# Performance work log

Measured on AMD Instinct MI355X. Metric: run time of the kernel, lower is better.

## Reference

```python
import jax, jax.numpy as jnp
import numpy as np
from math import factorial

LMAX = 8
BATCH = 65536


def _cg(j1, m1, j2, m2, j3, m3):
    """Clebsch-Gordan coefficient <j1 m1 j2 m2 | j3 m3> (Racah formula)."""
    if m1 + m2 != m3:
        return 0.0
    if j3 < abs(j1 - j2) or j3 > j1 + j2:
        return 0.0
    f = factorial
    pre = ((2 * j3 + 1) * f(j1 + j2 - j3) * f(j1 - j2 + j3) * f(-j1 + j2 + j3)
           / f(j1 + j2 + j3 + 1)) ** 0.5
    pre *= (f(j1 + m1) * f(j1 - m1) * f(j2 + m2) * f(j2 - m2)
            * f(j3 + m3) * f(j3 - m3)) ** 0.5
    kmin = max(0, j2 - j3 - m1, j1 - j3 + m2)
    kmax = min(j1 + j2 - j3, j1 - m1, j2 + m2)
    s = 0.0
    for k in range(kmin, kmax + 1):
        s += (-1) ** k / (f(k) * f(j1 + j2 - j3 - k) * f(j1 - m1 - k)
                          * f(j2 + m2 - k) * f(j3 - j2 + m1 + k) * f(j3 - j1 - m2 + k))
    return pre * s


def _cg_tensor(l1, l2, lo):
    C = np.zeros((2 * l1 + 1, 2 * l2 + 1, 2 * lo + 1), dtype=np.float32)
    for i, m1 in enumerate(range(-l1, l1 + 1)):
        for j, m2 in enumerate(range(-l2, l2 + 1)):
            M = m1 + m2
            if abs(M) <= lo:
                C[i, j, M + lo] = _cg(l1, m1, l2, m2, lo, M)
    return jnp.asarray(C)


def _build_full_index_map(lmax):
    im = []
    for l1 in range(lmax + 1):
        for l2 in range(l1, lmax + 1):
            for lv in range(abs(l1 - l2), min(l1 + l2, lmax) + 1):
                im.append((l1, l2, lv))
    return im


def _build_cg_power_index_map(lmax):
    if lmax < 2:
        return []
    entries = []
    for l2 in range(2, lmax + 1):
        lo_min = l2 - 1
        lo_max = min(l2 + 1, lmax)
        entries.append((1, l2, lo_min))
        if l2 >= 4 and lo_min + 1 <= lo_max:
            entries.append((1, l2, lo_min + 1))
    for l2 in range(3, lmax + 1):
        lo_min = l2 - 2
        lo_max = min(l2 + 2, lmax)
        entries.append((2, l2, lo_min))
        if lo_min + 1 <= lo_max:
            entries.append((2, l2, lo_min + 1))
    if lmax >= 3:
        entries.append((3, 3, 2))
    for l2 in range(4, lmax + 1):
        lo_min = l2 - 3
        lo_max = min(l2 + 3, lmax)
        entries.append((3, l2, lo_min))
        if l2 % 2 == 1 and l2 >= 5:
            if lo_min + 1 <= lo_max:
                entries.append((3, l2, lo_min + 1))
            if lo_min + 2 <= lo_max:
                entries.append((3, l2, lo_min + 2))
    return entries


FULL_MAP = _build_full_index_map(LMAX)
POWER_MAP = _build_cg_power_index_map(LMAX)
_CG = {t: _cg_tensor(*t) for t in sorted(set(FULL_MAP) | set(POWER_MAP))}
N_OUT = len(FULL_MAP) + len(POWER_MAP)


def setup_inputs() -> dict:
    k1, k2 = jax.random.split(jax.random.key(0))
    shape = (BATCH, LMAX + 1, LMAX + 1)
    return {
        "coeffs_real": jax.random.normal(k1, shape, dtype=jnp.float32),
        "coeffs_imag": jax.random.normal(k2, shape, dtype=jnp.float32),
    }


def _full_coeffs(c):
    """Extend m>=0 coefficients to full m range: F_l^{-m} = (-1)^m conj(F_l^m)."""
    F = {}
    for l in range(LMAX + 1):
        pos = c[:, l, :l + 1]  # (B, l+1), m = 0..l
        if l == 0:
            F[l] = pos
        else:
            signs = jnp.asarray((-1.0) ** np.arange(1, l + 1), dtype=jnp.float32)
            neg = (signs * jnp.conj(pos[:, 1:]))[:, ::-1]  # m = -l..-1
            F[l] = jnp.concatenate([neg, pos], axis=1)  # (B, 2l+1)
    return F


def reference(coeffs_real, coeffs_imag):
    c = (coeffs_real + 1j * coeffs_imag).astype(jnp.complex64)
    F = _full_coeffs(c)
    outs = []
    # scalar bispectrum entries: beta = sum_{m1,m2} C F1 F2 conj(F_lo^{m1+m2})
    for (l1, l2, lo) in FULL_MAP:
        C = _CG[(l1, l2, lo)]
        G = jnp.einsum('bi,bj,ijk->bk', F[l1], F[l2], C)  # coupled component, (B, 2lo+1)
        beta = jnp.sum(G * jnp.conj(F[lo]), axis=1)
        outs.append(beta.real)
    for (l1, l2, lo) in POWER_MAP:
        C = _CG[(l1, l2, lo)]
        G = jnp.einsum('bi,bj,ijk->bk', F[l1], F[l2], C)
        outs.append(jnp.sum(G.real ** 2 + G.imag ** 2, axis=1))
    return jnp.stack(outs, axis=1)  # (B, N_OUT) float32
```

## Files before the change

### kernel.cpp

```cpp
#include <hip/hip_runtime.h>
#include <utility>

#define LMAX 8
#define NENT 249
#define NPAIR 45
#define EPB 128
#define TPB 512
#define ESTR 130
#define NCO 45
#define PLANE (NCO*ESTR)
#define P1END 30
#define FSPLIT 100
#define PSLOT 115
#define NSLOT 149

typedef __attribute__((ext_vector_type(2))) float f32x2;

struct P2 { int l1, l2; };

__host__ __device__ constexpr int tri_(int l){ return l*(l+1)/2; }
__host__ __device__ constexpr int sr_(int m){ return m>=0 ? 1 : (((-m)&1)? -1 : 1); }
__host__ __device__ constexpr int sq_(int m){ return m>=0 ? 1 : (((-m)&1)? 1 : -1); }

__host__ __device__ constexpr P2 pair_of(int w){
  int n=0;
  for(int a=0;a<=LMAX;a++) for(int b=a;b<=LMAX;b++){ if(n==w) return P2{a,b}; n++; }
  return P2{0,0};
}

__host__ __device__ constexpr int full_rank(int l1,int l2,int lo){
  int r=0;
  for(int a=0;a<=LMAX;a++) for(int b=a;b<=LMAX;b++){
    int hi=a+b>LMAX?LMAX:a+b;
    for(int c=b-a;c<=hi;c++){ if(a==l1&&b==l2&&c==lo) return r; r++; }
  }
  return -1;
}

__host__ __device__ constexpr int power_idx(int l1,int l2,int lo){
  int n=0;
  for(int b=2;b<=LMAX;b++){
    if(l1==1&&l2==b&&lo==b-1) return n; n++;
    if(b>=4){ if(l1==1&&l2==b&&lo==b) return n; n++; }
  }
  for(int b=3;b<=LMAX;b++){
    if(l1==2&&l2==b&&lo==b-2) return n; n++;
    if(l1==2&&l2==b&&lo==b-1) return n; n++;
  }
  if(l1==3&&l2==3&&lo==2) return n; n++;
  for(int b=4;b<=LMAX;b++){
    if(l1==3&&l2==b&&lo==b-3) return n; n++;
    if((b&1)&&b>=5){
      if(l1==3&&l2==b&&lo==b-2) return n; n++;
      if(l1==3&&l2==b&&lo==b-1) return n; n++;
    }
  }
  return -1;
}

__host__ __device__ constexpr double csqrt_(double x){
  if (x<=0.0) return 0.0;
  double v=x, s=1.0;
  while (v>4.0){ v*=0.25; s*=2.0; }
  while (v<0.25){ v*=4.0; s*=0.5; }
  double g=v;
  for(int i=0;i<48;i++) g=0.5*(g+v/g);
  return g*s;
}
__host__ __device__ constexpr double cgC(int j1,int m1,int j2,int m2,int j3,int m3){
  if (m1+m2 != m3) return 0.0;
  int dj=j1-j2; if(dj<0)dj=-dj;
  if (j3<dj || j3>j1+j2) return 0.0;
  if (m2<-j2 || m2>j2 || m1<-j1 || m1>j1 || m3<-j3 || m3>j3) return 0.0;
  double f[26]={}; f[0]=1.0;
  for(int t=1;t<26;t++) f[t]=f[t-1]*(double)t;
  double pre = csqrt_((2.0*j3+1.0)*f[j1+j2-j3]*f[j1-j2+j3]*f[-j1+j2+j3]/f[j1+j2+j3+1]);
  pre *= csqrt_(f[j1+m1]*f[j1-m1]*f[j2+m2]*f[j2-m2]*f[j3+m3]*f[j3-m3]);
  int kmin=0; if(j2-j3-m1>kmin)kmin=j2-j3-m1; if(j1-j3+m2>kmin)kmin=j1-j3+m2;
  int kmax=j1+j2-j3; if(j1-m1<kmax)kmax=j1-m1; if(j2+m2<kmax)kmax=j2+m2;
  double s=0.0;
  for(int k=kmin;k<=kmax;k++){
    double term = 1.0/(f[k]*f[j1+j2-j3-k]*f[j1-m1-k]*f[j2+m2-k]*f[j3-j2+m1+k]*f[j3-j1-m2+k]);
    s += (k&1)? -term : term;
  }
  return pre*s;
}

template<int L1,int L2>
struct CGTab {
  static constexpr int LOmx = (L1+L2<LMAX)?(L1+L2):LMAX;
  static constexpr int LOmn = L2-L1;
  static constexpr int NLO  = LOmx-LOmn+1;
  float c[NLO][2*LOmx+1][2*L1+1];
};
template<int L1,int L2>
__host__ __device__ constexpr CGTab<L1,L2> make_cgtab(){
  CGTab<L1,L2> T{};
  for(int lo=T.LOmn; lo<=T.LOmx; lo++)
    for(int M=-T.LOmx; M<=T.LOmx; M++)
      for(int m1=-L1;m1<=L1;m1++){
        double v=0.0;
        if (M>=-lo && M<=lo){
          int m2=M-m1;
          if(m2>=-L2&&m2<=L2) v = cgC(L1,m1,L2,m2,lo,M);
        }
        T.c[lo-T.LOmn][M+T.LOmx][m1+L1] = (float)v;
      }
  return T;
}

template<int PI>
__device__ __attribute__((always_inline)) inline void do_pair(
    const float* __restrict__ lds, float* __restrict__ stage, int lane2)
{
  constexpr P2 pe = pair_of(PI);
  constexpr int L1 = pe.l1, L2 = pe.l2;
  constexpr int LOmin = L2-L1;
  constexpr int LOmax = (L1+L2<LMAX)?(L1+L2):LMAX;
  constexpr int NLO = LOmax-LOmin+1;
  constexpr int B1 = tri_(L1), B2 = tri_(L2);
  constexpr auto tab = make_cgtab<L1,L2>();

  f32x2 X1[L1+1], Y1[L1+1], X2[L2+1], Y2[L2+1];
#pragma unroll
  for (int a=0;a<=L1;a++){
    X1[a] = *(const f32x2*)&lds[(B1+a)*ESTR + lane2];
    Y1[a] = *(const f32x2*)&lds[PLANE + (B1+a)*ESTR + lane2];
  }
#pragma unroll
  for (int a=0;a<=L2;a++){
    X2[a] = *(const f32x2*)&lds[(B2+a)*ESTR + lane2];
    Y2[a] = *(const f32x2*)&lds[PLANE + (B2+a)*ESTR + lane2];
  }

  f32x2 bAcc[NLO], pAcc[NLO];
#pragma unroll
  for (int t=0;t<NLO;t++){ bAcc[t]=f32x2{0.f,0.f}; pAcc[t]=f32x2{0.f,0.f}; }

#pragma unroll
  for (int M=-LOmax; M<=LOmax; M++){
    const int m1lo = (M-L2 > -L1) ? (M-L2) : -L1;
    const int m1hi = (M+L2 <  L1) ? (M+L2) :  L1;
    f32x2 Prd[2*L1+1], Pid[2*L1+1];
#pragma unroll
    for (int m1=-L1; m1<=L1; m1++){
      if (m1<m1lo || m1>m1hi) continue;
      const int i  = m1-m1lo;
      const int m2 = M-m1;
      const int a1 = m1<0?-m1:m1, a2 = m2<0?-m2:m2;
      const int s1 = sr_(m1)*sr_(m2);
      const int s2 = -(sq_(m1)*sq_(m2));
      const int s3 = sr_(m1)*sq_(m2);
      const int s4 = sq_(m1)*sr_(m2);
      f32x2 t1 = (s1>0? X1[a1] : -X1[a1]) * X2[a2];
      Prd[i] = __builtin_elementwise_fma((s2>0? Y1[a1] : -Y1[a1]), Y2[a2], t1);
      f32x2 t2 = (s3>0? X1[a1] : -X1[a1]) * Y2[a2];
      Pid[i] = __builtin_elementwise_fma((s4>0? Y1[a1] : -Y1[a1]), X2[a2], t2);
    }
#pragma unroll
    for (int lo=LOmin; lo<=LOmax; lo++){
      if (lo < (M<0?-M:M)) continue;
      f32x2 Gr = {0.f,0.f}, Gi = {0.f,0.f};
#pragma unroll
      for (int m1=-L1; m1<=L1; m1++){
        if (m1<m1lo || m1>m1hi) continue;
        const int i = m1-m1lo;
        const float C = tab.c[lo-LOmin][M+LOmax][m1+L1];
        if (C != 0.f){
          f32x2 Cv = {C,C};
          Gr = __builtin_elementwise_fma(Cv, Prd[i], Gr);
          Gi = __builtin_elementwise_fma(Cv, Pid[i], Gi);
        }
      }
      const int aM = M<0?-M:M;
      const int B3 = tri_(lo);
      f32x2 x3 = *(const f32x2*)&lds[(B3+aM)*ESTR + lane2];
      f32x2 y3 = *(const f32x2*)&lds[PLANE + (B3+aM)*ESTR + lane2];
      const int AL = sr_(M), BE = sq_(M);
      bAcc[lo-LOmin] = __builtin_elementwise_fma(Gr, (AL>0? x3 : -x3), bAcc[lo-LOmin]);
      bAcc[lo-LOmin] = __builtin_elementwise_fma(Gi, (BE>0? y3 : -y3), bAcc[lo-LOmin]);
      if (power_idx(L1,L2,lo) >= 0){
        pAcc[lo-LOmin] = __builtin_elementwise_fma(Gr, Gr, pAcc[lo-LOmin]);
        pAcc[lo-LOmin] = __builtin_elementwise_fma(Gi, Gi, pAcc[lo-LOmin]);
      }
    }
  }

#pragma unroll
  for (int lo=LOmin; lo<=LOmax; lo++){
    const int fr   = full_rank(L1,L2,lo);
    const int slot = fr<FSPLIT ? fr : fr-FSPLIT;
    *(f32x2*)&stage[slot*ESTR + lane2] = bAcc[lo-LOmin];
    const int pidx = power_idx(L1,L2,lo);
    if (pidx>=0)
      *(f32x2*)&stage[(PSLOT+pidx)*ESTR + lane2] = pAcc[lo-LOmin];
  }
}

template<int PI>
__device__ __attribute__((always_inline)) inline void pair_step(
    const float* __restrict__ lds, float* __restrict__ stage, int lane2, int s, int e_)
{
  if (PI>=s && PI<e_) do_pair<PI>(lds, stage, lane2);
}
template<int OFF, int... Ps>
__device__ __attribute__((always_inline)) inline void pair_range(
    std::integer_sequence<int,Ps...>,
    const float* __restrict__ lds, float* __restrict__ stage, int lane2, int s, int e_)
{
  (pair_step<OFF+Ps>(lds, stage, lane2, s, e_), ...);
}

struct Bnd { int e1[8]; int e2[8]; };

constexpr int LDS_FLOATS = 2*PLANE + NSLOT*ESTR;
constexpr int LDS_BYTES  = LDS_FLOATS*4;
static_assert(LDS_BYTES <= 160*1024, "LDS over 160KB");

__global__ __launch_bounds__(TPB, 2) void main_kernel(
    const float* __restrict__ re, const float* __restrict__ im,
    float* __restrict__ out, Bnd bnd)
{
  extern __shared__ float lds[];
  float* stage = lds + 2*PLANE;
  const int gbase = blockIdx.x*EPB;

  for (int t=threadIdx.x; t<EPB*81; t+=TPB){
    float vr = re[(size_t)gbase*81 + t];
    float vi = im[(size_t)gbase*81 + t];
    int elem = t/81, x = t - elem*81;
    int l = x/9, m = x - l*9;
    if (m<=l){
      int off = tri_(l)+m;
      lds[off*ESTR+elem] = vr;
      lds[PLANE + off*ESTR+elem] = vi;
    }
  }
  __syncthreads();

  const int lane  = threadIdx.x & 63;
  const int wv    = __builtin_amdgcn_readfirstlane(threadIdx.x >> 6);
  const int lane2 = lane*2;
  const int s1 = (wv==0)? 0      : bnd.e1[wv-1];
  const int E1 = bnd.e1[wv];
  const int s2 = (wv==0)? P1END  : bnd.e2[wv-1];
  const int E2 = bnd.e2[wv];
  const long long obase = (long long)gbase*NENT;

  pair_range<0>(std::make_integer_sequence<int,P1END>{}, lds, stage, lane2, s1, E1);
  __syncthreads();

  for (int p=threadIdx.x; p<EPB*FSPLIT; p+=TPB){
    int elem = p/FSPLIT, o = p - elem*FSPLIT;
    out[obase + (long long)elem*NENT + o] = stage[o*ESTR + elem];
  }
  __syncthreads();

  pair_range<P1END>(std::make_integer_sequence<int,NPAIR-P1END>{}, lds, stage, lane2, s2, E2);
  __syncthreads();

  for (int p=threadIdx.x; p<EPB*NSLOT; p+=TPB){
    int elem = p/NSLOT, o = p - elem*NSLOT;
    out[obase + (long long)elem*NENT + FSPLIT + o] = stage[o*ESTR + elem];
  }
}

extern "C" void kernel_launch(void* const* d_in, const int* in_sizes, int n_in,
                              void* d_out, int out_size, void* d_ws, size_t ws_size,
                              hipStream_t stream) {
  const float* re = (const float*)d_in[0];
  const float* im = (const float*)d_in[1];
  float* out = (float*)d_out;
  const int batch = in_sizes[0] / 81;

  hipFuncSetAttribute((const void*)main_kernel,
                      hipFuncAttributeMaxDynamicSharedMemorySize, LDS_BYTES);

  double w[NPAIR];
  for (int p=0;p<NPAIR;p++){
    P2 pe = pair_of(p);
    int L1=pe.l1, L2=pe.l2;
    int LOmx=(L1+L2<LMAX)?(L1+L2):LMAX, LOmn=L2-L1;
    double ww = 2.0*(L1+L2+2);
    for (int M=-LOmx;M<=LOmx;M++){
      int lo_ = (M-L2>-L1)?(M-L2):-L1, hi_ = (M+L2<L1)?(M+L2):L1;
      int dn = hi_-lo_+1;
      ww += 4.0*dn;
      int aM = M<0?-M:M;
      for (int lo=(LOmn>aM?LOmn:aM); lo<=LOmx; lo++)
        ww += 2.0*dn + 2.0 + (power_idx(L1,L2,lo)>=0 ? 2.0 : 0.0);
    }
    w[p]=ww;
  }
  Bnd bnd;
  {
    double tot=0; for(int p=0;p<P1END;p++) tot+=w[p];
    double acc=0; int c=0;
    for(int p=0;p<P1END && c<7;p++){ acc+=w[p]; if(acc>=tot*(c+1)/8.0) bnd.e1[c++]=p+1; }
    while(c<7) bnd.e1[c++]=P1END;
    bnd.e1[7]=P1END;
  }
  {
    double tot=0; for(int p=P1END;p<NPAIR;p++) tot+=w[p];
    double acc=0; int c=0;
    for(int p=P1END;p<NPAIR && c<7;p++){ acc+=w[p]; if(acc>=tot*(c+1)/8.0) bnd.e2[c++]=p+1; }
    while(c<7) bnd.e2[c++]=NPAIR;
    bnd.e2[7]=NPAIR;
  }

  main_kernel<<<batch/EPB, TPB, LDS_BYTES, stream>>>(re, im, out, bnd);
}
```

Measured before the change: 369.3 us.

## Use 16 waves per block and split heavy pairs by M parity with LDS atomics

Doubles the block to 1024 threads (16 waves) and splits expensive coupling pairs into two work units, one for even M and one for odd M, so the work can be balanced across more waves. The split units accumulate into the LDS stage buffer with atomicAdd, which requires zeroing the stage before each phase. The aim is to cut per-wave critical-path time through finer load balancing. It adds LDS atomic traffic, extra zeroing passes and register pressure under the tighter launch bound (1024 threads, 4 blocks).

Measured after the change: 1.011 ms. 2.74x slower.

```diff
diff --git a/kernel.cpp b/kernel.cpp
--- a/kernel.cpp
+++ b/kernel.cpp
@@ -5,7 +5,8 @@
 #define NENT 249
 #define NPAIR 45
 #define EPB 128
-#define TPB 512
+#define TPB 1024
+#define NWV 16
 #define ESTR 130
 #define NCO 45
 #define PLANE (NCO*ESTR)
@@ -56,6 +57,43 @@
     }
   }
   return -1;
+}
+
+__host__ __device__ constexpr double pair_w(int p){
+  P2 pe = pair_of(p);
+  int L1=pe.l1, L2=pe.l2;
+  int LOmx=(L1+L2<LMAX)?(L1+L2):LMAX, LOmn=L2-L1;
+  double ww = 2.0*(L1+L2+2);
+  for (int M=-LOmx;M<=LOmx;M++){
+    int lo_ = (M-L2>-L1)?(M-L2):-L1, hi_ = (M+L2<L1)?(M+L2):L1;
+    int dn = hi_-lo_+1;
+    ww += 4.0*dn;
+    int aM = M<0?-M:M;
+    for (int lo=(LOmn>aM?LOmn:aM); lo<=LOmx; lo++)
+      ww += 2.0*dn + 2.0 + (power_idx(L1,L2,lo)>=0 ? 2.0 : 0.0);
+  }
+  return ww;
+}
+__host__ __device__ constexpr bool is_split(int p){ return pair_w(p) > 1000.0; }
+
+__host__ __device__ constexpr int n_units(){
+  int n=0; for(int p=0;p<NPAIR;p++) n += is_split(p)?2:1; return n;
+}
+__host__ __device__ constexpr int p1_units(){
+  int n=0; for(int p=0;p<P1END;p++) n += is_split(p)?2:1; return n;
+}
+constexpr int NUNIT = n_units();
+constexpr int P1U   = p1_units();
+
+__host__ __device__ constexpr int unit_pair(int u){
+  int n=0;
+  for(int p=0;p<NPAIR;p++){ int c=is_split(p)?2:1; if(u<n+c) return p; n+=c; }
+  return NPAIR-1;
+}
+__host__ __device__ constexpr int unit_part(int u){
+  int n=0;
+  for(int p=0;p<NPAIR;p++){ int c=is_split(p)?2:1; if(u<n+c) return is_split(p)?(u-n+1):0; n+=c; }
+  return 0;
 }
 
 __host__ __device__ constexpr double csqrt_(double x){
@@ -109,7 +147,7 @@
   return T;
 }
 
-template<int PI>
+template<int PI, int PART>
 __device__ __attribute__((always_inline)) inline void do_pair(
     const float* __restrict__ lds, float* __restrict__ stage, int lane2)
 {
@@ -139,6 +177,8 @@
 
 #pragma unroll
   for (int M=-LOmax; M<=LOmax; M++){
+    if (PART==1 && (M&1)) continue;
+    if (PART==2 && !(M&1)) continue;
     const int m1lo = (M-L2 > -L1) ? (M-L2) : -L1;
     const int m1hi = (M+L2 <  L1) ? (M+L2) :  L1;
     f32x2 Prd[2*L1+1], Pid[2*L1+1];
@@ -190,40 +230,47 @@
   for (int lo=LOmin; lo<=LOmax; lo++){
     const int fr   = full_rank(L1,L2,lo);
     const int slot = fr<FSPLIT ? fr : fr-FSPLIT;
-    *(f32x2*)&stage[slot*ESTR + lane2] = bAcc[lo-LOmin];
+    float* bp = &stage[slot*ESTR + lane2];
+    if (PART==0) *(f32x2*)bp = bAcc[lo-LOmin];
+    else { atomicAdd(bp, bAcc[lo-LOmin][0]); atomicAdd(bp+1, bAcc[lo-LOmin][1]); }
     const int pidx = power_idx(L1,L2,lo);
-    if (pidx>=0)
-      *(f32x2*)&stage[(PSLOT+pidx)*ESTR + lane2] = pAcc[lo-LOmin];
-  }
-}
-
-template<int PI>
-__device__ __attribute__((always_inline)) inline void pair_step(
+    if (pidx>=0){
+      float* pp = &stage[(PSLOT+pidx)*ESTR + lane2];
+      if (PART==0) *(f32x2*)pp = pAcc[lo-LOmin];
+      else { atomicAdd(pp, pAcc[lo-LOmin][0]); atomicAdd(pp+1, pAcc[lo-LOmin][1]); }
+    }
+  }
+}
+
+template<int U>
+__device__ __attribute__((always_inline)) inline void unit_step(
     const float* __restrict__ lds, float* __restrict__ stage, int lane2, int s, int e_)
 {
-  if (PI>=s && PI<e_) do_pair<PI>(lds, stage, lane2);
-}
-template<int OFF, int... Ps>
-__device__ __attribute__((always_inline)) inline void pair_range(
-    std::integer_sequence<int,Ps...>,
+  if (U>=s && U<e_) do_pair<unit_pair(U), unit_part(U)>(lds, stage, lane2);
+}
+template<int OFF, int... Us>
+__device__ __attribute__((always_inline)) inline void unit_range(
+    std::integer_sequence<int,Us...>,
     const float* __restrict__ lds, float* __restrict__ stage, int lane2, int s, int e_)
 {
-  (pair_step<OFF+Ps>(lds, stage, lane2, s, e_), ...);
-}
-
-struct Bnd { int e1[8]; int e2[8]; };
+  (unit_step<OFF+Us>(lds, stage, lane2, s, e_), ...);
+}
+
+struct Bnd { int e1[NWV]; int e2[NWV]; };
 
 constexpr int LDS_FLOATS = 2*PLANE + NSLOT*ESTR;
 constexpr int LDS_BYTES  = LDS_FLOATS*4;
 static_assert(LDS_BYTES <= 160*1024, "LDS over 160KB");
 
-__global__ __launch_bounds__(TPB, 2) void main_kernel(
+__global__ __launch_bounds__(TPB, 4) void main_kernel(
     const float* __restrict__ re, const float* __restrict__ im,
     float* __restrict__ out, Bnd bnd)
 {
   extern __shared__ float lds[];
   float* stage = lds + 2*PLANE;
   const int gbase = blockIdx.x*EPB;
+
+  for (int t=threadIdx.x; t<NSLOT*ESTR; t+=TPB) stage[t]=0.f;
 
   for (int t=threadIdx.x; t<EPB*81; t+=TPB){
     float vr = re[(size_t)gbase*81 + t];
@@ -241,22 +288,25 @@
   const int lane  = threadIdx.x & 63;
   const int wv    = __builtin_amdgcn_readfirstlane(threadIdx.x >> 6);
   const int lane2 = lane*2;
-  const int s1 = (wv==0)? 0      : bnd.e1[wv-1];
+  const int s1 = (wv==0)? 0    : bnd.e1[wv-1];
   const int E1 = bnd.e1[wv];
-  const int s2 = (wv==0)? P1END  : bnd.e2[wv-1];
+  const int s2 = (wv==0)? P1U  : bnd.e2[wv-1];
   const int E2 = bnd.e2[wv];
   const long long obase = (long long)gbase*NENT;
 
-  pair_range<0>(std::make_integer_sequence<int,P1END>{}, lds, stage, lane2, s1, E1);
+  unit_range<0>(std::make_integer_sequence<int,P1U>{}, lds, stage, lane2, s1, E1);
   __syncthreads();
 
-  for (int p=threadIdx.x; p<EPB*FSPLIT; p+=TPB){
-    int elem = p/FSPLIT, o = p - elem*FSPLIT;
-    out[obase + (long long)elem*NENT + o] = stage[o*ESTR + elem];
+  for (int p=threadIdx.x; p<EPB*PSLOT; p+=TPB){
+    int elem = p/PSLOT, o = p - elem*PSLOT;
+    float v = stage[o*ESTR + elem];
+    stage[o*ESTR + elem] = 0.f;
+    if (o < FSPLIT)
+      out[obase + (long long)elem*NENT + o] = v;
   }
   __syncthreads();
 
-  pair_range<P1END>(std::make_integer_sequence<int,NPAIR-P1END>{}, lds, stage, lane2, s2, E2);
+  unit_range<P1U>(std::make_integer_sequence<int,NUNIT-P1U>{}, lds, stage, lane2, s2, E2);
   __syncthreads();
 
   for (int p=threadIdx.x; p<EPB*NSLOT; p+=TPB){
@@ -276,36 +326,35 @@
   hipFuncSetAttribute((const void*)main_kernel,
                       hipFuncAttributeMaxDynamicSharedMemorySize, LDS_BYTES);
 
-  double w[NPAIR];
-  for (int p=0;p<NPAIR;p++){
-    P2 pe = pair_of(p);
-    int L1=pe.l1, L2=pe.l2;
-    int LOmx=(L1+L2<LMAX)?(L1+L2):LMAX, LOmn=L2-L1;
-    double ww = 2.0*(L1+L2+2);
-    for (int M=-LOmx;M<=LOmx;M++){
-      int lo_ = (M-L2>-L1)?(M-L2):-L1, hi_ = (M+L2<L1)?(M+L2):L1;
-      int dn = hi_-lo_+1;
-      ww += 4.0*dn;
-      int aM = M<0?-M:M;
-      for (int lo=(LOmn>aM?LOmn:aM); lo<=LOmx; lo++)
-        ww += 2.0*dn + 2.0 + (power_idx(L1,L2,lo)>=0 ? 2.0 : 0.0);
-    }
-    w[p]=ww;
+  double uw[NUNIT];
+  {
+    int n=0;
+    for (int p=0;p<NPAIR;p++){
+      double w = pair_w(p);
+      if (is_split(p)){ uw[n++]=w*0.5; uw[n++]=w*0.5; }
+      else            { uw[n++]=w; }
+    }
   }
   Bnd bnd;
   {
-    double tot=0; for(int p=0;p<P1END;p++) tot+=w[p];
+    double tot=0; for(int u=0;u<P1U;u++) tot+=uw[u];
     double acc=0; int c=0;
-    for(int p=0;p<P1END && c<7;p++){ acc+=w[p]; if(acc>=tot*(c+1)/8.0) bnd.e1[c++]=p+1; }
-    while(c<7) bnd.e1[c++]=P1END;
-    bnd.e1[7]=P1END;
+    for(int u=0;u<P1U && c<NWV-1;u++){
+      acc+=uw[u];
+      while(c<NWV-1 && acc>=tot*(c+1)/(double)NWV) bnd.e1[c++]=u+1;
+    }
+    while(c<NWV-1) bnd.e1[c++]=P1U;
+    bnd.e1[NWV-1]=P1U;
   }
   {
-    double tot=0; for(int p=P1END;p<NPAIR;p++) tot+=w[p];
+    double tot=0; for(int u=P1U;u<NUNIT;u++) tot+=uw[u];
     double acc=0; int c=0;
-    for(int p=P1END;p<NPAIR && c<7;p++){ acc+=w[p]; if(acc>=tot*(c+1)/8.0) bnd.e2[c++]=p+1; }
-    while(c<7) bnd.e2[c++]=NPAIR;
-    bnd.e2[7]=NPAIR;
+    for(int u=P1U;u<NUNIT && c<NWV-1;u++){
+      acc+=uw[u];
+      while(c<NWV-1 && acc>=tot*(c+1)/(double)NWV) bnd.e2[c++]=u+1;
+    }
+    while(c<NWV-1) bnd.e2[c++]=NUNIT;
+    bnd.e2[NWV-1]=NUNIT;
   }
 
   main_kernel<<<batch/EPB, TPB, LDS_BYTES, stream>>>(re, im, out, bnd);
```

## Split heavy pairs into m1 chunks and balance units across waves with greedy masks

Applied to the files above, without the earlier changes.

Pairs with l1>=6 in the second phase are split into two chunks over |m1|. Each chunk accumulates its partial bispectrum into LDS with atomicAdd, and the stage slots are zeroed after the first flush. Work units are no longer contiguous pair ranges: the host assigns them to waves through a longest-processing-time greedy bitmask, to reduce imbalance between the 8 waves. This costs LDS atomics, extra recomputation of the G terms per chunk, and a larger unrolled code body. The launch_bounds minimum-blocks hint of 2 is also dropped.

After: 538.0 us. +45.7%, slower.

```diff
diff --git a/kernel.cpp b/kernel.cpp
--- a/kernel.cpp
+++ b/kernel.cpp
@@ -56,6 +56,53 @@
     }
   }
   return -1;
+}
+
+__host__ __device__ constexpr bool is_sp(int p){ return pair_of(p).l1 >= 6; }
+__host__ __device__ constexpr bool in_ck(int CK,int L1,int m1){
+  int a = m1<0?-m1:m1;
+  return CK==0 || (CK==1 ? (a<=L1/2) : (a>L1/2));
+}
+__host__ __device__ constexpr int ck_dn(int CK,int L1,int L2,int M){
+  int lo = (M-L2>-L1)?(M-L2):-L1, hi = (M+L2<L1)?(M+L2):L1;
+  int n=0; for(int m1=lo;m1<=hi;m1++) if(in_ck(CK,L1,m1)) n++;
+  return n;
+}
+
+__host__ __device__ constexpr int n_units(){
+  int n=P1END;
+  for(int p=P1END;p<NPAIR;p++) n += is_sp(p)?2:1;
+  return n;
+}
+constexpr int NUNITS = n_units();
+
+__host__ __device__ constexpr int unit_pair(int u){
+  if (u<P1END) return u;
+  int n=P1END;
+  for(int p=P1END;p<NPAIR;p++){ int c=is_sp(p)?2:1; if(u<n+c) return p; n+=c; }
+  return NPAIR-1;
+}
+__host__ __device__ constexpr int unit_chunk(int u){
+  if (u<P1END) return 0;
+  int n=P1END;
+  for(int p=P1END;p<NPAIR;p++){ int c=is_sp(p)?2:1; if(u<n+c) return is_sp(p)?(u-n+1):0; n+=c; }
+  return 0;
+}
+
+__host__ double pair_w_ck(int p,int ck){
+  P2 pe = pair_of(p);
+  int L1=pe.l1, L2=pe.l2;
+  int LOmx=(L1+L2<LMAX)?(L1+L2):LMAX, LOmn=L2-L1;
+  double ww = 2.0*(L1+L2+2);
+  for (int M=-LOmx;M<=LOmx;M++){
+    int dn = ck_dn(ck,L1,L2,M);
+    if (!dn) continue;
+    ww += 4.0*dn;
+    int aM = M<0?-M:M;
+    for (int lo=(LOmn>aM?LOmn:aM); lo<=LOmx; lo++)
+      ww += 2.0*dn + 2.0 + (power_idx(L1,L2,lo)>=0 ? 2.0 : 0.0);
+  }
+  return ww;
 }
 
 __host__ __device__ constexpr double csqrt_(double x){
@@ -109,7 +156,7 @@
   return T;
 }
 
-template<int PI>
+template<int PI, int CK>
 __device__ __attribute__((always_inline)) inline void do_pair(
     const float* __restrict__ lds, float* __restrict__ stage, int lane2)
 {
@@ -119,11 +166,14 @@
   constexpr int LOmax = (L1+L2<LMAX)?(L1+L2):LMAX;
   constexpr int NLO = LOmax-LOmin+1;
   constexpr int B1 = tri_(L1), B2 = tri_(L2);
+  constexpr int AH = L1/2;
   constexpr auto tab = make_cgtab<L1,L2>();
 
   f32x2 X1[L1+1], Y1[L1+1], X2[L2+1], Y2[L2+1];
 #pragma unroll
   for (int a=0;a<=L1;a++){
+    if (CK==1 && a>AH) continue;
+    if (CK==2 && a<=AH) continue;
     X1[a] = *(const f32x2*)&lds[(B1+a)*ESTR + lane2];
     Y1[a] = *(const f32x2*)&lds[PLANE + (B1+a)*ESTR + lane2];
   }
@@ -139,13 +189,14 @@
 
 #pragma unroll
   for (int M=-LOmax; M<=LOmax; M++){
+    if (ck_dn(CK,L1,L2,M)==0) continue;
     const int m1lo = (M-L2 > -L1) ? (M-L2) : -L1;
     const int m1hi = (M+L2 <  L1) ? (M+L2) :  L1;
     f32x2 Prd[2*L1+1], Pid[2*L1+1];
 #pragma unroll
     for (int m1=-L1; m1<=L1; m1++){
       if (m1<m1lo || m1>m1hi) continue;
-      const int i  = m1-m1lo;
+      if (!in_ck(CK,L1,m1)) continue;
       const int m2 = M-m1;
       const int a1 = m1<0?-m1:m1, a2 = m2<0?-m2:m2;
       const int s1 = sr_(m1)*sr_(m2);
@@ -153,35 +204,39 @@
       const int s3 = sr_(m1)*sq_(m2);
       const int s4 = sq_(m1)*sr_(m2);
       f32x2 t1 = (s1>0? X1[a1] : -X1[a1]) * X2[a2];
-      Prd[i] = __builtin_elementwise_fma((s2>0? Y1[a1] : -Y1[a1]), Y2[a2], t1);
+      Prd[m1+L1] = __builtin_elementwise_fma((s2>0? Y1[a1] : -Y1[a1]), Y2[a2], t1);
       f32x2 t2 = (s3>0? X1[a1] : -X1[a1]) * Y2[a2];
-      Pid[i] = __builtin_elementwise_fma((s4>0? Y1[a1] : -Y1[a1]), X2[a2], t2);
+      Pid[m1+L1] = __builtin_elementwise_fma((s4>0? Y1[a1] : -Y1[a1]), X2[a2], t2);
     }
 #pragma unroll
     for (int lo=LOmin; lo<=LOmax; lo++){
       if (lo < (M<0?-M:M)) continue;
       f32x2 Gr = {0.f,0.f}, Gi = {0.f,0.f};
+      bool used = false;
 #pragma unroll
       for (int m1=-L1; m1<=L1; m1++){
         if (m1<m1lo || m1>m1hi) continue;
-        const int i = m1-m1lo;
+        if (!in_ck(CK,L1,m1)) continue;
         const float C = tab.c[lo-LOmin][M+LOmax][m1+L1];
         if (C != 0.f){
+          used = true;
           f32x2 Cv = {C,C};
-          Gr = __builtin_elementwise_fma(Cv, Prd[i], Gr);
-          Gi = __builtin_elementwise_fma(Cv, Pid[i], Gi);
+          Gr = __builtin_elementwise_fma(Cv, Prd[m1+L1], Gr);
+          Gi = __builtin_elementwise_fma(Cv, Pid[m1+L1], Gi);
         }
       }
-      const int aM = M<0?-M:M;
-      const int B3 = tri_(lo);
-      f32x2 x3 = *(const f32x2*)&lds[(B3+aM)*ESTR + lane2];
-      f32x2 y3 = *(const f32x2*)&lds[PLANE + (B3+aM)*ESTR + lane2];
-      const int AL = sr_(M), BE = sq_(M);
-      bAcc[lo-LOmin] = __builtin_elementwise_fma(Gr, (AL>0? x3 : -x3), bAcc[lo-LOmin]);
-      bAcc[lo-LOmin] = __builtin_elementwise_fma(Gi, (BE>0? y3 : -y3), bAcc[lo-LOmin]);
-      if (power_idx(L1,L2,lo) >= 0){
-        pAcc[lo-LOmin] = __builtin_elementwise_fma(Gr, Gr, pAcc[lo-LOmin]);
-        pAcc[lo-LOmin] = __builtin_elementwise_fma(Gi, Gi, pAcc[lo-LOmin]);
+      if (used){
+        const int aM = M<0?-M:M;
+        const int B3 = tri_(lo);
+        f32x2 x3 = *(const f32x2*)&lds[(B3+aM)*ESTR + lane2];
+        f32x2 y3 = *(const f32x2*)&lds[PLANE + (B3+aM)*ESTR + lane2];
+        const int AL = sr_(M), BE = sq_(M);
+        bAcc[lo-LOmin] = __builtin_elementwise_fma(Gr, (AL>0? x3 : -x3), bAcc[lo-LOmin]);
+        bAcc[lo-LOmin] = __builtin_elementwise_fma(Gi, (BE>0? y3 : -y3), bAcc[lo-LOmin]);
+        if (power_idx(L1,L2,lo) >= 0){
+          pAcc[lo-LOmin] = __builtin_elementwise_fma(Gr, Gr, pAcc[lo-LOmin]);
+          pAcc[lo-LOmin] = __builtin_elementwise_fma(Gi, Gi, pAcc[lo-LOmin]);
+        }
       }
     }
   }
@@ -190,36 +245,43 @@
   for (int lo=LOmin; lo<=LOmax; lo++){
     const int fr   = full_rank(L1,L2,lo);
     const int slot = fr<FSPLIT ? fr : fr-FSPLIT;
-    *(f32x2*)&stage[slot*ESTR + lane2] = bAcc[lo-LOmin];
     const int pidx = power_idx(L1,L2,lo);
-    if (pidx>=0)
-      *(f32x2*)&stage[(PSLOT+pidx)*ESTR + lane2] = pAcc[lo-LOmin];
-  }
-}
-
-template<int PI>
-__device__ __attribute__((always_inline)) inline void pair_step(
-    const float* __restrict__ lds, float* __restrict__ stage, int lane2, int s, int e_)
+    if (CK==0){
+      *(f32x2*)&stage[slot*ESTR + lane2] = bAcc[lo-LOmin];
+      if (pidx>=0)
+        *(f32x2*)&stage[(PSLOT+pidx)*ESTR + lane2] = pAcc[lo-LOmin];
+    } else {
+      atomicAdd(&stage[slot*ESTR + lane2],     bAcc[lo-LOmin][0]);
+      atomicAdd(&stage[slot*ESTR + lane2 + 1], bAcc[lo-LOmin][1]);
+    }
+  }
+}
+
+template<int U>
+__device__ __attribute__((always_inline)) inline void unit_step(
+    const float* __restrict__ lds, float* __restrict__ stage, int lane2,
+    unsigned long long mk)
 {
-  if (PI>=s && PI<e_) do_pair<PI>(lds, stage, lane2);
-}
-template<int OFF, int... Ps>
-__device__ __attribute__((always_inline)) inline void pair_range(
-    std::integer_sequence<int,Ps...>,
-    const float* __restrict__ lds, float* __restrict__ stage, int lane2, int s, int e_)
+  if ((mk>>U)&1ull) do_pair<unit_pair(U), unit_chunk(U)>(lds, stage, lane2);
+}
+template<int OFF, int... Us>
+__device__ __attribute__((always_inline)) inline void unit_range(
+    std::integer_sequence<int,Us...>,
+    const float* __restrict__ lds, float* __restrict__ stage, int lane2,
+    unsigned long long mk)
 {
-  (pair_step<OFF+Ps>(lds, stage, lane2, s, e_), ...);
-}
-
-struct Bnd { int e1[8]; int e2[8]; };
+  (unit_step<OFF+Us>(lds, stage, lane2, mk), ...);
+}
+
+struct Msk { unsigned long long m[8]; };
 
 constexpr int LDS_FLOATS = 2*PLANE + NSLOT*ESTR;
 constexpr int LDS_BYTES  = LDS_FLOATS*4;
 static_assert(LDS_BYTES <= 160*1024, "LDS over 160KB");
 
-__global__ __launch_bounds__(TPB, 2) void main_kernel(
+__global__ __launch_bounds__(TPB) void main_kernel(
     const float* __restrict__ re, const float* __restrict__ im,
-    float* __restrict__ out, Bnd bnd)
+    float* __restrict__ out, Msk msk)
 {
   extern __shared__ float lds[];
   float* stage = lds + 2*PLANE;
@@ -241,22 +303,23 @@
   const int lane  = threadIdx.x & 63;
   const int wv    = __builtin_amdgcn_readfirstlane(threadIdx.x >> 6);
   const int lane2 = lane*2;
-  const int s1 = (wv==0)? 0      : bnd.e1[wv-1];
-  const int E1 = bnd.e1[wv];
-  const int s2 = (wv==0)? P1END  : bnd.e2[wv-1];
-  const int E2 = bnd.e2[wv];
+  const unsigned long long mk = msk.m[wv];
   const long long obase = (long long)gbase*NENT;
 
-  pair_range<0>(std::make_integer_sequence<int,P1END>{}, lds, stage, lane2, s1, E1);
+  unit_range<0>(std::make_integer_sequence<int,P1END>{}, lds, stage, lane2, mk);
   __syncthreads();
 
-  for (int p=threadIdx.x; p<EPB*FSPLIT; p+=TPB){
-    int elem = p/FSPLIT, o = p - elem*FSPLIT;
-    out[obase + (long long)elem*NENT + o] = stage[o*ESTR + elem];
+  for (int p=threadIdx.x; p<EPB*PSLOT; p+=TPB){
+    int elem = p/PSLOT, o = p - elem*PSLOT;
+    float v = stage[o*ESTR + elem];
+    stage[o*ESTR + elem] = 0.f;
+    if (o < FSPLIT)
+      out[obase + (long long)elem*NENT + o] = v;
   }
   __syncthreads();
 
-  pair_range<P1END>(std::make_integer_sequence<int,NPAIR-P1END>{}, lds, stage, lane2, s2, E2);
+  unit_range<P1END>(std::make_integer_sequence<int,NUNITS-P1END>{},
+                    lds, stage, lane2, mk);
   __syncthreads();
 
   for (int p=threadIdx.x; p<EPB*NSLOT; p+=TPB){
@@ -276,37 +339,30 @@
   hipFuncSetAttribute((const void*)main_kernel,
                       hipFuncAttributeMaxDynamicSharedMemorySize, LDS_BYTES);
 
-  double w[NPAIR];
-  for (int p=0;p<NPAIR;p++){
-    P2 pe = pair_of(p);
-    int L1=pe.l1, L2=pe.l2;
-    int LOmx=(L1+L2<LMAX)?(L1+L2):LMAX, LOmn=L2-L1;
-    double ww = 2.0*(L1+L2+2);
-    for (int M=-LOmx;M<=LOmx;M++){
-      int lo_ = (M-L2>-L1)?(M-L2):-L1, hi_ = (M+L2<L1)?(M+L2):L1;
-      int dn = hi_-lo_+1;
-      ww += 4.0*dn;
-      int aM = M<0?-M:M;
-      for (int lo=(LOmn>aM?LOmn:aM); lo<=LOmx; lo++)
-        ww += 2.0*dn + 2.0 + (power_idx(L1,L2,lo)>=0 ? 2.0 : 0.0);
-    }
-    w[p]=ww;
-  }
-  Bnd bnd;
+  Msk msk{};
   {
-    double tot=0; for(int p=0;p<P1END;p++) tot+=w[p];
-    double acc=0; int c=0;
-    for(int p=0;p<P1END && c<7;p++){ acc+=w[p]; if(acc>=tot*(c+1)/8.0) bnd.e1[c++]=p+1; }
-    while(c<7) bnd.e1[c++]=P1END;
-    bnd.e1[7]=P1END;
-  }
-  {
-    double tot=0; for(int p=P1END;p<NPAIR;p++) tot+=w[p];
-    double acc=0; int c=0;
-    for(int p=P1END;p<NPAIR && c<7;p++){ acc+=w[p]; if(acc>=tot*(c+1)/8.0) bnd.e2[c++]=p+1; }
-    while(c<7) bnd.e2[c++]=NPAIR;
-    bnd.e2[7]=NPAIR;
-  }
-
-  main_kernel<<<batch/EPB, TPB, LDS_BYTES, stream>>>(re, im, out, bnd);
-}
+    double uw[NUNITS]; int order[NUNITS];
+    for (int u=0;u<NUNITS;u++){
+      uw[u] = pair_w_ck(unit_pair(u), unit_chunk(u));
+      order[u] = u;
+    }
+    for (int i=0;i<NUNITS;i++){
+      int mx=i;
+      for (int j=i+1;j<NUNITS;j++) if (uw[order[j]]>uw[order[mx]]) mx=j;
+      int t=order[i]; order[i]=order[mx]; order[mx]=t;
+    }
+    double loadA[8]={}, loadB[8]={};
+    for (int i=0;i<NUNITS;i++){
+      int u = order[i];
+      if (u < P1END){
+        int b=0; for (int j=1;j<8;j++) if (loadA[j]<loadA[b]) b=j;
+        msk.m[b] |= 1ull<<u; loadA[b] += uw[u];
+      } else {
+        int b=0; for (int j=1;j<8;j++) if (loadB[j]<loadB[b]) b=j;
+        msk.m[b] |= 1ull<<u; loadB[b] += uw[u];
+      }
+    }
+  }
+
+  main_kernel<<<batch/EPB, TPB, LDS_BYTES, stream>>>(re, im, out, msk);
+}
```
